# Kernel tuning notes

Hardware: AMD Instinct MI355X
Metric: run time of the kernel (lower is better)

Reference implementation:

```python
import jax, jax.numpy as jnp
import numpy as np

NUM_HEADS = 2
ROPE_BASE = 10000.0


def _rope_tables(seq_len, head_dim, dtype):
    # inv_freq over even indices of head_dim
    inv_freq = 1.0 / (ROPE_BASE ** (jnp.arange(0, head_dim, 2, dtype=jnp.float32) / head_dim))
    t = jnp.arange(seq_len, dtype=jnp.float32)
    freqs = t[:, None] * inv_freq[None, :]            # (s, head_dim/2)
    emb = jnp.concatenate([freqs, freqs], axis=-1)    # (s, head_dim)
    return jnp.cos(emb).astype(dtype), jnp.sin(emb).astype(dtype)


def _apply_rotation(x_bsd, cos, sin):
    # x_bsd: (b, s, h*d); chunk in half along last dim (h=2 -> halves == head_dim)
    x1, x2 = jnp.split(x_bsd, 2, axis=-1)
    return jnp.concatenate([x1 * cos - x2 * sin, x2 * cos + x1 * sin], axis=-1)


def setup_inputs() -> dict:
    key = jax.random.key(0)
    k1, k2, k3, k4 = jax.random.split(key, 4)
    b, s, dim = 4, 2048, 2048
    x = jax.random.normal(k1, (b, s, dim), dtype=jnp.float32)
    wqkv = jax.random.normal(k2, (dim, 3 * dim), dtype=jnp.float32) * (dim ** -0.5)
    wout = jax.random.normal(k3, (dim, dim), dtype=jnp.float32) * (dim ** -0.5)
    bout = jax.random.normal(k4, (dim,), dtype=jnp.float32) * 0.01
    return {"x": x, "wqkv": wqkv, "wout": wout, "bout": bout}


def reference(x, wqkv, wout, bout):
    b, s, dim = x.shape
    h = NUM_HEADS
    d = dim // h
    scale = d ** -0.5

    qkv = x @ wqkv                                    # (b, s, 3*dim)
    qkv = qkv.reshape(b, s, 3, h, d).transpose(2, 0, 3, 1, 4)  # (3, b, h, s, d)
    q, k, v = qkv[0], qkv[1], qkv[2]                  # (b, h, s, d)

    # RoPE applied on (b, s, h*d) layout, exactly as source
    cos, sin = _rope_tables(s, d, x.dtype)            # (s, d) each
    q_flat = q.transpose(0, 2, 1, 3).reshape(b, s, h * d)
    k_flat = k.transpose(0, 2, 1, 3).reshape(b, s, h * d)
    q = _apply_rotation(q_flat, cos, sin).reshape(b, s, h, d).transpose(0, 2, 1, 3)
    k = _apply_rotation(k_flat, cos, sin).reshape(b, s, h, d).transpose(0, 2, 1, 3)

    scores = jnp.einsum('bhid,bhjd->bhij', q, k) * scale
    attn = jax.nn.softmax(scores, axis=-1)
    out = jnp.einsum('bhij,bhjd->bhid', attn, v)      # (b, h, s, d)
    out = out.transpose(0, 2, 1, 3).reshape(b, s, dim)
    return out @ wout + bout
```

## Files before the change

kernel.cpp:

```cpp
#include <hip/hip_runtime.h>
#include <hip/hip_fp16.h>

typedef __attribute__((ext_vector_type(4))) float f32x4;
typedef __attribute__((ext_vector_type(8))) _Float16 f16x8;
typedef __attribute__((ext_vector_type(4))) _Float16 f16x4;

__device__ __forceinline__ void gload_lds16(const void* gp, void* lp) {
    __builtin_amdgcn_global_load_lds(
        (const __attribute__((address_space(1))) void*)gp,
        (__attribute__((address_space(3))) void*)lp, 16, 0, 0);
}

__global__ void rope_tables_k(float* __restrict__ cosT, float* __restrict__ sinT) {
    int idx = blockIdx.x * 256 + threadIdx.x;
    int s = idx >> 9, j = idx & 511;
    float invf = exp2f(-13.287712379549449f * (float)j * (1.0f / 512.0f));
    float ang = (float)s * invf;
    float sn, cs;
    sincosf(ang, &sn, &cs);
    cosT[idx] = cs;
    sinT[idx] = sn;
}

__global__ void f32_to_f16_vec(const float* __restrict__ in, _Float16* __restrict__ out) {
    long i = ((long)blockIdx.x * 256 + threadIdx.x) * 4;
    f32x4 v = *(const f32x4*)(in + i);
    f16x4 h;
#pragma unroll
    for (int e = 0; e < 4; ++e) h[e] = (_Float16)v[e];
    *(f16x4*)(out + i) = h;
}

__global__ void transpose_f32_to_f16(const float* __restrict__ in, _Float16* __restrict__ out,
                                     int R, int C) {
    __shared__ _Float16 tile[32][36];
    const int c0 = blockIdx.x * 32, r0 = blockIdx.y * 32;
    const int t = threadIdx.x;
    const int r = t >> 3, c4 = (t & 7) * 4;
    f32x4 v = *(const f32x4*)(in + (long)(r0 + r) * C + c0 + c4);
    f16x4 h;
#pragma unroll
    for (int e = 0; e < 4; ++e) h[e] = (_Float16)v[e];
    *(f16x4*)&tile[r][c4] = h;
    __syncthreads();
    const int oc = t >> 3, o4 = (t & 7) * 4;
    f16x4 o;
#pragma unroll
    for (int e = 0; e < 4; ++e) o[e] = tile[o4 + e][oc];
    *(f16x4*)(out + (long)(c0 + oc) * R + r0 + o4) = o;
}

__global__ void rope_inplace(_Float16* __restrict__ qkv, const float* __restrict__ cosT,
                             const float* __restrict__ sinT) {
    const int row = blockIdx.x;
    const int s = row & 2047;
    const int j0 = threadIdx.x * 4;
    _Float16* base = qkv + (long)row * 6144;
    f16x4 q0 = *(const f16x4*)(base + j0);
    f16x4 q1 = *(const f16x4*)(base + 1024 + j0);
    f16x4 k0 = *(const f16x4*)(base + 2048 + j0);
    f16x4 k1 = *(const f16x4*)(base + 3072 + j0);
    const int jj = j0 & 511;
    f32x4 cs = *(const f32x4*)(cosT + (long)s * 512 + jj);
    f32x4 sn = *(const f32x4*)(sinT + (long)s * 512 + jj);
    f16x4 oq0, oq1, ok0, ok1;
#pragma unroll
    for (int e = 0; e < 4; ++e) {
        float a = (float)q0[e], b = (float)q1[e];
        oq0[e] = (_Float16)(a * cs[e] - b * sn[e]);
        oq1[e] = (_Float16)(b * cs[e] + a * sn[e]);
        float c = (float)k0[e], d = (float)k1[e];
        ok0[e] = (_Float16)(c * cs[e] - d * sn[e]);
        ok1[e] = (_Float16)(d * cs[e] + c * sn[e]);
    }
    *(f16x4*)(base + j0) = oq0;
    *(f16x4*)(base + 1024 + j0) = oq1;
    *(f16x4*)(base + 2048 + j0) = ok0;
    *(f16x4*)(base + 3072 + j0) = ok1;
}

__global__ void v_transpose(const _Float16* __restrict__ qkv, _Float16* __restrict__ vT) {
    __shared__ _Float16 tile[32][36];
    const int z = blockIdx.z, b = z >> 1, h = z & 1;
    const int s0 = blockIdx.x * 32, d0 = blockIdx.y * 32;
    const int t = threadIdx.x;
    const int r = t >> 3, c4 = (t & 7) * 4;
    const _Float16* src = qkv + (long)(b * 2048 + s0 + r) * 6144 + 4096 + h * 1024 + d0 + c4;
    *(f16x4*)&tile[r][c4] = *(const f16x4*)src;
    __syncthreads();
    const int dr = t >> 3, sc = (t & 7) * 4;
    f16x4 o;
#pragma unroll
    for (int e = 0; e < 4; ++e) o[e] = tile[sc + e][dr];
    *(f16x4*)(vT + ((long)z * 1024 + d0 + dr) * 2048 + s0 + sc) = o;
}

__global__ __launch_bounds__(256) void softmax_rows_f32(float* __restrict__ S, float scale) {
    const int wid = threadIdx.x >> 6, lane = threadIdx.x & 63;
    const long row = (long)blockIdx.x * 4 + wid;
    float* rp = S + row * 2048;
    f32x4 v[8];
    float mx = -1e30f;
#pragma unroll
    for (int i = 0; i < 8; ++i) {
        v[i] = *(const f32x4*)(rp + (i * 64 + lane) * 4);
#pragma unroll
        for (int e = 0; e < 4; ++e) mx = fmaxf(mx, v[i][e]);
    }
#pragma unroll
    for (int o = 32; o > 0; o >>= 1) mx = fmaxf(mx, __shfl_xor(mx, o, 64));
    float sum = 0.f;
#pragma unroll
    for (int i = 0; i < 8; ++i)
#pragma unroll
        for (int e = 0; e < 4; ++e) {
            float p = __expf(scale * (v[i][e] - mx));
            v[i][e] = p; sum += p;
        }
#pragma unroll
    for (int o = 32; o > 0; o >>= 1) sum += __shfl_xor(sum, o, 64);
    float inv = 1.0f / sum;
    _Float16* wp = (_Float16*)S + row * 4096;
#pragma unroll
    for (int i = 0; i < 8; ++i) {
        f16x4 h;
#pragma unroll
        for (int e = 0; e < 4; ++e) h[e] = (_Float16)(v[i][e] * inv);
        *(f16x4*)(wp + (i * 64 + lane) * 4) = h;
    }
}

__global__ __launch_bounds__(256) void softmax_rows_f16(_Float16* __restrict__ S, float scale) {
    const int wid = threadIdx.x >> 6, lane = threadIdx.x & 63;
    const long row = (long)blockIdx.x * 4 + wid;
    _Float16* rp = S + row * 2048;
    f16x8 v[4];
    float f[32];
    float mx = -1e30f;
#pragma unroll
    for (int i = 0; i < 4; ++i) {
        v[i] = *(const f16x8*)(rp + i * 512 + lane * 8);
#pragma unroll
        for (int e = 0; e < 8; ++e) {
            f[i * 8 + e] = (float)v[i][e];
            mx = fmaxf(mx, f[i * 8 + e]);
        }
    }
#pragma unroll
    for (int o = 32; o > 0; o >>= 1) mx = fmaxf(mx, __shfl_xor(mx, o, 64));
    float sum = 0.f;
#pragma unroll
    for (int i = 0; i < 32; ++i) {
        float p = __expf(scale * (f[i] - mx));
        f[i] = p; sum += p;
    }
#pragma unroll
    for (int o = 32; o > 0; o >>= 1) sum += __shfl_xor(sum, o, 64);
    float inv = 1.0f / sum;
#pragma unroll
    for (int i = 0; i < 4; ++i) {
        f16x8 h;
#pragma unroll
        for (int e = 0; e < 8; ++e) h[e] = (_Float16)(f[i * 8 + e] * inv);
        *(f16x8*)(rp + i * 512 + lane * 8) = h;
    }
}

template <bool OUT_F16, bool BIAS>
__global__ __launch_bounds__(256, 2)
void gemm_rg(const _Float16* __restrict__ A, const _Float16* __restrict__ B,
             void* __restrict__ Cv, const float* __restrict__ bias,
             int K, int lda, int ldb, int ldc, int zmod,
             long a1, long a2, long b1, long b2, long c1, long c2) {
    __shared__ char lds[73728];
    const int z = blockIdx.z, zq = z / zmod, zr = z - zq * zmod;
    A += zq * a1 + zr * a2;
    B += zq * b1 + zr * b2;
    const long coff = zq * c1 + zr * c2;
    const int tm = blockIdx.y * 256, tn = blockIdx.x * 128;
    const int t = threadIdx.x;
    const int lane = t & 63, wid = t >> 6;
    const int wr = wid >> 1, wc = wid & 1;
    const int fr = lane & 15, kg = lane >> 4;

    const int strow = t >> 2;
    const int stcol = 8 * ((t & 3) ^ ((t >> 3) & 3));
    const _Float16* gA = A + (long)(tm + strow) * lda + stcol;
    const _Float16* gB = B + (long)(tn + strow) * ldb + stcol;
    const int ldsw = wid * 1024;

    const int swz = 16 * (kg ^ ((fr >> 1) & 3));
    const int arow = (wr * 128 + fr) * 64 + swz;
    const int brow = 16384 + (wc * 64 + fr) * 64 + swz;

    const int NT = K >> 5;
    f32x4 acc[8][4] = {};

    auto stage = [&](int tt, int slot) {
        const long ko = (long)tt * 32;
        char* d = lds + slot * 24576 + ldsw;
#pragma unroll
        for (int i = 0; i < 4; ++i)
            gload_lds16(gA + ko + (long)(i * 64) * lda, d + i * 4096);
#pragma unroll
        for (int i = 0; i < 2; ++i)
            gload_lds16(gB + ko + (long)(i * 64) * ldb, d + 16384 + i * 4096);
    };

    stage(0, 0);
    stage(1, 1);

    int st = 0, sp = 2;
    for (int tt = 0; tt < NT; ++tt) {
        if (tt + 1 < NT) asm volatile("s_waitcnt vmcnt(6)" ::: "memory");
        else             asm volatile("s_waitcnt vmcnt(0)" ::: "memory");
        __builtin_amdgcn_s_barrier();
        const char* buf = lds + st * 24576;
        f16x8 af[8], bf[4];
#pragma unroll
        for (int m = 0; m < 8; ++m) af[m] = *(const f16x8*)(buf + arow + m * 1024);
#pragma unroll
        for (int n = 0; n < 4; ++n) bf[n] = *(const f16x8*)(buf + brow + n * 1024);
        if (tt + 2 < NT) stage(tt + 2, sp);
        __builtin_amdgcn_s_setprio(1);
#pragma unroll
        for (int m = 0; m < 8; ++m)
#pragma unroll
            for (int n = 0; n < 4; ++n)
                acc[m][n] = __builtin_amdgcn_mfma_f32_16x16x32_f16(af[m], bf[n], acc[m][n], 0, 0, 0);
        __builtin_amdgcn_s_setprio(0);
        st = (st == 2) ? 0 : st + 1;
        sp = (sp == 2) ? 0 : sp + 1;
    }

    const int rb = tm + wr * 128 + (lane >> 4) * 4;
    const int cb = tn + wc * 64 + fr;
#pragma unroll
    for (int m = 0; m < 8; ++m) {
#pragma unroll
        for (int n = 0; n < 4; ++n) {
#pragma unroll
            for (int r = 0; r < 4; ++r) {
                float v = acc[m][n][r];
                const int row = rb + m * 16 + r;
                const int col = cb + n * 16;
                if (BIAS) v += bias[col];
                if (OUT_F16)
                    ((_Float16*)Cv)[coff + (long)row * ldc + col] = (_Float16)v;
                else
                    ((float*)Cv)[coff + (long)row * ldc + col] = v;
            }
        }
    }
}

extern "C" void kernel_launch(void* const* d_in, const int* in_sizes, int n_in,
                              void* d_out, int out_size, void* d_ws, size_t ws_size,
                              hipStream_t stream) {
    const float* x    = (const float*)d_in[0];
    const float* wqkv = (const float*)d_in[1];
    const float* wout = (const float*)d_in[2];
    const float* bout = (const float*)d_in[3];
    char* ws = (char*)d_ws;

    _Float16* qkv_h = (_Float16*)(ws);
    _Float16* x_h   = (_Float16*)(ws + 100663296);
    _Float16* wqkvT = (_Float16*)(ws + 134217728);
    _Float16* vT    = (_Float16*)(ws + 100663296);
    float*    cosT  = (float*)(ws + 100663296);
    float*    sinT  = (float*)(ws + 104857600);
    _Float16* woutT = (_Float16*)(ws);
    const bool batched = ws_size >= 234881024ULL;

    f32_to_f16_vec<<<dim3(16384), dim3(256), 0, stream>>>(x, x_h);
    transpose_f32_to_f16<<<dim3(192, 64), dim3(256), 0, stream>>>(wqkv, wqkvT, 2048, 6144);
    gemm_rg<true, false><<<dim3(48, 32, 1), dim3(256), 0, stream>>>(
        x_h, wqkvT, (void*)qkv_h, nullptr, 2048, 2048, 2048, 6144,
        1, 0L, 0L, 0L, 0L, 0L, 0L);
    rope_tables_k<<<dim3(4096), dim3(256), 0, stream>>>(cosT, sinT);
    rope_inplace<<<dim3(8192), dim3(256), 0, stream>>>(qkv_h, cosT, sinT);
    v_transpose<<<dim3(64, 32, 8), dim3(256), 0, stream>>>(qkv_h, vT);

    if (batched) {
        _Float16* S16  = (_Float16*)(ws + 134217728);
        _Float16* aout = (_Float16*)(ws + 201326592);
        gemm_rg<true, false><<<dim3(16, 8, 8), dim3(256), 0, stream>>>(
            qkv_h, qkv_h + 2048, (void*)S16, nullptr, 1024, 6144, 6144, 2048,
            2, 12582912L, 1024L, 12582912L, 1024L, 8388608L, 4194304L);
        softmax_rows_f16<<<dim3(4096), dim3(256), 0, stream>>>(S16, 0.03125f);
        gemm_rg<true, false><<<dim3(8, 8, 8), dim3(256), 0, stream>>>(
            S16, vT, (void*)aout, nullptr, 2048, 2048, 2048, 2048,
            2, 8388608L, 4194304L, 4194304L, 2097152L, 4194304L, 1024L);
        transpose_f32_to_f16<<<dim3(64, 64), dim3(256), 0, stream>>>(wout, woutT, 2048, 2048);
        gemm_rg<false, true><<<dim3(16, 32, 1), dim3(256), 0, stream>>>(
            aout, woutT, d_out, bout, 2048, 2048, 2048, 2048,
            1, 0L, 0L, 0L, 0L, 0L, 0L);
    } else {
        float*    S32  = (float*)(ws + 134217728);
        _Float16* aout = (_Float16*)(ws + 150994944);
        for (int z = 0; z < 8; ++z) {
            const _Float16* Az = qkv_h + (long)(z >> 1) * 12582912 + (z & 1) * 1024;
            gemm_rg<false, false><<<dim3(16, 8, 1), dim3(256), 0, stream>>>(
                Az, Az + 2048, (void*)S32, nullptr, 1024, 6144, 6144, 2048,
                1, 0L, 0L, 0L, 0L, 0L, 0L);
            softmax_rows_f32<<<dim3(512), dim3(256), 0, stream>>>(S32, 0.03125f);
            gemm_rg<true, false><<<dim3(8, 8, 1), dim3(256), 0, stream>>>(
                (const _Float16*)S32, vT + (long)z * 2097152,
                (void*)(aout + (long)(z >> 1) * 4194304 + (z & 1) * 1024), nullptr,
                2048, 4096, 2048, 2048, 1, 0L, 0L, 0L, 0L, 0L, 0L);
        }
        transpose_f32_to_f16<<<dim3(64, 64), dim3(256), 0, stream>>>(wout, woutT, 2048, 2048);
        gemm_rg<false, true><<<dim3(16, 32, 1), dim3(256), 0, stream>>>(
            aout, woutT, d_out, bout, 2048, 2048, 2048, 2048,
            1, 0L, 0L, 0L, 0L, 0L, 0L);
    }
}
```

Before: 565.8 us.

## Switch GEMMs to 32x32x16 MFMA and fold softmax exp/normalize into GEMM epilogues

```diff
diff --git a/kernel.cpp b/kernel.cpp
--- a/kernel.cpp
+++ b/kernel.cpp
@@ -2,6 +2,7 @@
 #include <hip/hip_fp16.h>
 
 typedef __attribute__((ext_vector_type(4))) float f32x4;
+typedef __attribute__((ext_vector_type(16))) float f32x16;
 typedef __attribute__((ext_vector_type(8))) _Float16 f16x8;
 typedef __attribute__((ext_vector_type(4))) _Float16 f16x4;
 
@@ -9,6 +10,10 @@
     __builtin_amdgcn_global_load_lds(
         (const __attribute__((address_space(1))) void*)gp,
         (__attribute__((address_space(3))) void*)lp, 16, 0, 0);
+}
+
+__device__ __forceinline__ void barrier_fenced() {
+    asm volatile("s_barrier" ::: "memory");
 }
 
 __global__ void rope_tables_k(float* __restrict__ cosT, float* __restrict__ sinT) {
@@ -130,48 +135,29 @@
     }
 }
 
-__global__ __launch_bounds__(256) void softmax_rows_f16(_Float16* __restrict__ S, float scale) {
+__global__ __launch_bounds__(256) void rowsum_f16(const _Float16* __restrict__ S,
+                                                  float* __restrict__ l) {
     const int wid = threadIdx.x >> 6, lane = threadIdx.x & 63;
     const long row = (long)blockIdx.x * 4 + wid;
-    _Float16* rp = S + row * 2048;
-    f16x8 v[4];
-    float f[32];
-    float mx = -1e30f;
+    const _Float16* rp = S + row * 2048;
+    float sum = 0.f;
 #pragma unroll
     for (int i = 0; i < 4; ++i) {
-        v[i] = *(const f16x8*)(rp + i * 512 + lane * 8);
-#pragma unroll
-        for (int e = 0; e < 8; ++e) {
-            f[i * 8 + e] = (float)v[i][e];
-            mx = fmaxf(mx, f[i * 8 + e]);
-        }
-    }
-#pragma unroll
-    for (int o = 32; o > 0; o >>= 1) mx = fmaxf(mx, __shfl_xor(mx, o, 64));
-    float sum = 0.f;
-#pragma unroll
-    for (int i = 0; i < 32; ++i) {
-        float p = __expf(scale * (f[i] - mx));
-        f[i] = p; sum += p;
+        f16x8 v = *(const f16x8*)(rp + i * 512 + lane * 8);
+#pragma unroll
+        for (int e = 0; e < 8; ++e) sum += (float)v[e];
     }
 #pragma unroll
     for (int o = 32; o > 0; o >>= 1) sum += __shfl_xor(sum, o, 64);
-    float inv = 1.0f / sum;
-#pragma unroll
-    for (int i = 0; i < 4; ++i) {
-        f16x8 h;
-#pragma unroll
-        for (int e = 0; e < 8; ++e) h[e] = (_Float16)(f[i * 8 + e] * inv);
-        *(f16x8*)(rp + i * 512 + lane * 8) = h;
-    }
-}
-
-template <bool OUT_F16, bool BIAS>
+    if (lane == 0) l[row] = sum;
+}
+
+template <int OMODE, bool BIAS>
 __global__ __launch_bounds__(256, 2)
-void gemm_rg(const _Float16* __restrict__ A, const _Float16* __restrict__ B,
-             void* __restrict__ Cv, const float* __restrict__ bias,
-             int K, int lda, int ldb, int ldc, int zmod,
-             long a1, long a2, long b1, long b2, long c1, long c2) {
+void gemm32(const _Float16* __restrict__ A, const _Float16* __restrict__ B,
+            void* __restrict__ Cv, const float* __restrict__ aux, float scale,
+            int K, int lda, int ldb, int ldc, int zmod,
+            long a1, long a2, long b1, long b2, long c1, long c2) {
     __shared__ char lds[73728];
     const int z = blockIdx.z, zq = z / zmod, zr = z - zq * zmod;
     A += zq * a1 + zr * a2;
@@ -181,20 +167,21 @@
     const int t = threadIdx.x;
     const int lane = t & 63, wid = t >> 6;
     const int wr = wid >> 1, wc = wid & 1;
-    const int fr = lane & 15, kg = lane >> 4;
+    const int l31 = lane & 31, kg = lane >> 5, l3 = lane & 3;
 
     const int strow = t >> 2;
-    const int stcol = 8 * ((t & 3) ^ ((t >> 3) & 3));
+    const int stcol = 8 * ((t & 3) ^ ((t >> 2) & 3));
     const _Float16* gA = A + (long)(tm + strow) * lda + stcol;
     const _Float16* gB = B + (long)(tn + strow) * ldb + stcol;
     const int ldsw = wid * 1024;
 
-    const int swz = 16 * (kg ^ ((fr >> 1) & 3));
-    const int arow = (wr * 128 + fr) * 64 + swz;
-    const int brow = 16384 + (wc * 64 + fr) * 64 + swz;
+    const int sw0 = 16 * ((0 + kg) ^ l3);
+    const int sw1 = 16 * ((2 + kg) ^ l3);
+    const int abase = (wr * 128 + l31) * 64;
+    const int bbase = 16384 + (wc * 64 + l31) * 64;
 
     const int NT = K >> 5;
-    f32x4 acc[8][4] = {};
+    f32x16 acc[4][2] = {};
 
     auto stage = [&](int tt, int slot) {
         const long ko = (long)tt * 32;
@@ -214,41 +201,56 @@
     for (int tt = 0; tt < NT; ++tt) {
         if (tt + 1 < NT) asm volatile("s_waitcnt vmcnt(6)" ::: "memory");
         else             asm volatile("s_waitcnt vmcnt(0)" ::: "memory");
-        __builtin_amdgcn_s_barrier();
+        barrier_fenced();
         const char* buf = lds + st * 24576;
-        f16x8 af[8], bf[4];
-#pragma unroll
-        for (int m = 0; m < 8; ++m) af[m] = *(const f16x8*)(buf + arow + m * 1024);
-#pragma unroll
-        for (int n = 0; n < 4; ++n) bf[n] = *(const f16x8*)(buf + brow + n * 1024);
+        f16x8 af[4][2], bf[2][2];
+#pragma unroll
+        for (int m = 0; m < 4; ++m) {
+            af[m][0] = *(const f16x8*)(buf + abase + m * 2048 + sw0);
+            af[m][1] = *(const f16x8*)(buf + abase + m * 2048 + sw1);
+        }
+#pragma unroll
+        for (int n = 0; n < 2; ++n) {
+            bf[n][0] = *(const f16x8*)(buf + bbase + n * 2048 + sw0);
+            bf[n][1] = *(const f16x8*)(buf + bbase + n * 2048 + sw1);
+        }
         if (tt + 2 < NT) stage(tt + 2, sp);
         __builtin_amdgcn_s_setprio(1);
 #pragma unroll
-        for (int m = 0; m < 8; ++m)
-#pragma unroll
-            for (int n = 0; n < 4; ++n)
-                acc[m][n] = __builtin_amdgcn_mfma_f32_16x16x32_f16(af[m], bf[n], acc[m][n], 0, 0, 0);
+        for (int ks = 0; ks < 2; ++ks)
+#pragma unroll
+            for (int m = 0; m < 4; ++m)
+#pragma unroll
+                for (int n = 0; n < 2; ++n)
+                    acc[m][n] = __builtin_amdgcn_mfma_f32_32x32x16_f16(af[m][ks], bf[n][ks], acc[m][n], 0, 0, 0);
         __builtin_amdgcn_s_setprio(0);
         st = (st == 2) ? 0 : st + 1;
         sp = (sp == 2) ? 0 : sp + 1;
     }
 
-    const int rb = tm + wr * 128 + (lane >> 4) * 4;
-    const int cb = tn + wc * 64 + fr;
-#pragma unroll
-    for (int m = 0; m < 8; ++m) {
-#pragma unroll
-        for (int n = 0; n < 4; ++n) {
-#pragma unroll
-            for (int r = 0; r < 4; ++r) {
+    const int rb = tm + wr * 128;
+    const int cb = tn + wc * 64 + l31;
+    const float* auxz = (OMODE == 3) ? (aux + (long)z * 2048) : aux;
+#pragma unroll
+    for (int m = 0; m < 4; ++m) {
+#pragma unroll
+        for (int r = 0; r < 16; ++r) {
+            const int rloc = (r & 3) + 8 * (r >> 2) + 4 * kg;
+            const int row = rb + m * 32 + rloc;
+            float inv = 1.0f;
+            if (OMODE == 3) inv = __builtin_amdgcn_rcpf(auxz[row]);
+#pragma unroll
+            for (int n = 0; n < 2; ++n) {
                 float v = acc[m][n][r];
-                const int row = rb + m * 16 + r;
-                const int col = cb + n * 16;
-                if (BIAS) v += bias[col];
-                if (OUT_F16)
+                const int col = cb + n * 32;
+                if (BIAS) v += aux[col];
+                if (OMODE == 0) {
+                    ((float*)Cv)[coff + (long)row * ldc + col] = v;
+                } else {
+                    if (OMODE == 2) v = __expf(v * scale);
+                    if (OMODE == 3) v *= inv;
                     ((_Float16*)Cv)[coff + (long)row * ldc + col] = (_Float16)v;
-                else
-                    ((float*)Cv)[coff + (long)row * ldc + col] = v;
+                }
             }
         }
     }
@@ -270,12 +272,12 @@
     float*    cosT  = (float*)(ws + 100663296);
     float*    sinT  = (float*)(ws + 104857600);
     _Float16* woutT = (_Float16*)(ws);
-    const bool batched = ws_size >= 234881024ULL;
+    const bool batched = ws_size >= 234946560ULL;
 
     f32_to_f16_vec<<<dim3(16384), dim3(256), 0, stream>>>(x, x_h);
     transpose_f32_to_f16<<<dim3(192, 64), dim3(256), 0, stream>>>(wqkv, wqkvT, 2048, 6144);
-    gemm_rg<true, false><<<dim3(48, 32, 1), dim3(256), 0, stream>>>(
-        x_h, wqkvT, (void*)qkv_h, nullptr, 2048, 2048, 2048, 6144,
+    gemm32<1, false><<<dim3(48, 32, 1), dim3(256), 0, stream>>>(
+        x_h, wqkvT, (void*)qkv_h, nullptr, 0.f, 2048, 2048, 2048, 6144,
         1, 0L, 0L, 0L, 0L, 0L, 0L);
     rope_tables_k<<<dim3(4096), dim3(256), 0, stream>>>(cosT, sinT);
     rope_inplace<<<dim3(8192), dim3(256), 0, stream>>>(qkv_h, cosT, sinT);
@@ -284,34 +286,35 @@
     if (batched) {
         _Float16* S16  = (_Float16*)(ws + 134217728);
         _Float16* aout = (_Float16*)(ws + 201326592);
-        gemm_rg<true, false><<<dim3(16, 8, 8), dim3(256), 0, stream>>>(
-            qkv_h, qkv_h + 2048, (void*)S16, nullptr, 1024, 6144, 6144, 2048,
+        float*    lsum = (float*)(ws + 234881024);
+        gemm32<2, false><<<dim3(16, 8, 8), dim3(256), 0, stream>>>(
+            qkv_h, qkv_h + 2048, (void*)S16, nullptr, 0.03125f, 1024, 6144, 6144, 2048,
             2, 12582912L, 1024L, 12582912L, 1024L, 8388608L, 4194304L);
-        softmax_rows_f16<<<dim3(4096), dim3(256), 0, stream>>>(S16, 0.03125f);
-        gemm_rg<true, false><<<dim3(8, 8, 8), dim3(256), 0, stream>>>(
-            S16, vT, (void*)aout, nullptr, 2048, 2048, 2048, 2048,
+        rowsum_f16<<<dim3(4096), dim3(256), 0, stream>>>(S16, lsum);
+        gemm32<3, false><<<dim3(8, 8, 8), dim3(256), 0, stream>>>(
+            S16, vT, (void*)aout, lsum, 0.f, 2048, 2048, 2048, 2048,
             2, 8388608L, 4194304L, 4194304L, 2097152L, 4194304L, 1024L);
         transpose_f32_to_f16<<<dim3(64, 64), dim3(256), 0, stream>>>(wout, woutT, 2048, 2048);
-        gemm_rg<false, true><<<dim3(16, 32, 1), dim3(256), 0, stream>>>(
-            aout, woutT, d_out, bout, 2048, 2048, 2048, 2048,
+        gemm32<0, true><<<dim3(16, 32, 1), dim3(256), 0, stream>>>(
+            aout, woutT, d_out, bout, 0.f, 2048, 2048, 2048, 2048,
             1, 0L, 0L, 0L, 0L, 0L, 0L);
     } else {
         float*    S32  = (float*)(ws + 134217728);
         _Float16* aout = (_Float16*)(ws + 150994944);
         for (int z = 0; z < 8; ++z) {
             const _Float16* Az = qkv_h + (long)(z >> 1) * 12582912 + (z & 1) * 1024;
-            gemm_rg<false, false><<<dim3(16, 8, 1), dim3(256), 0, stream>>>(
-                Az, Az + 2048, (void*)S32, nullptr, 1024, 6144, 6144, 2048,
+            gemm32<0, false><<<dim3(16, 8, 1), dim3(256), 0, stream>>>(
+                Az, Az + 2048, (void*)S32, nullptr, 0.f, 1024, 6144, 6144, 2048,
                 1, 0L, 0L, 0L, 0L, 0L, 0L);
             softmax_rows_f32<<<dim3(512), dim3(256), 0, stream>>>(S32, 0.03125f);
-            gemm_rg<true, false><<<dim3(8, 8, 1), dim3(256), 0, stream>>>(
+            gemm32<1, false><<<dim3(8, 8, 1), dim3(256), 0, stream>>>(
                 (const _Float16*)S32, vT + (long)z * 2097152,
-                (void*)(aout + (long)(z >> 1) * 4194304 + (z & 1) * 1024), nullptr,
+                (void*)(aout + (long)(z >> 1) * 4194304 + (z & 1) * 1024), nullptr, 0.f,
                 2048, 4096, 2048, 2048, 1, 0L, 0L, 0L, 0L, 0L, 0L);
         }
         transpose_f32_to_f16<<<dim3(64, 64), dim3(256), 0, stream>>>(wout, woutT, 2048, 2048);
-        gemm_rg<false, true><<<dim3(16, 32, 1), dim3(256), 0, stream>>>(
-            aout, woutT, d_out, bout, 2048, 2048, 2048, 2048,
+        gemm32<0, true><<<dim3(16, 32, 1), dim3(256), 0, stream>>>(
+            aout, woutT, d_out, bout, 0.f, 2048, 2048, 2048, 2048,
             1, 0L, 0L, 0L, 0L, 0L, 0L);
     }
 }
```

New measurement: 582.5 us. +3.0%, slower.
